# Kernel tuning notes

Measured on AMD Instinct MI355X. Metric: run time of the kernel, lower is better.

## Reference

```python
import jax, jax.numpy as jnp
import numpy as np

D_MODEL = 1024
NUM_HEADS = 16
D_K = D_MODEL // NUM_HEADS


def setup_inputs() -> dict:
    key = jax.random.key(0)
    ks = jax.random.split(key, 7)
    B, S = 4, 2048
    lim = float(np.sqrt(6.0 / (D_MODEL + D_MODEL)))  # xavier uniform
    x = jax.random.normal(ks[0], (B, S, D_MODEL), dtype=jnp.float32)
    w_q = jax.random.uniform(ks[1], (D_MODEL, D_MODEL), jnp.float32, -lim, lim)
    w_k = jax.random.uniform(ks[2], (D_MODEL, D_MODEL), jnp.float32, -lim, lim)
    w_v = jax.random.uniform(ks[3], (D_MODEL, D_MODEL), jnp.float32, -lim, lim)
    w_o = jax.random.uniform(ks[4], (D_MODEL, D_MODEL), jnp.float32, -lim, lim)
    b_o = jnp.zeros((D_MODEL,), jnp.float32)
    ln_g = jnp.ones((D_MODEL,), jnp.float32)
    ln_b = jnp.zeros((D_MODEL,), jnp.float32)
    return {"x": x, "w_q": w_q, "w_k": w_k, "w_v": w_v, "w_o": w_o,
            "b_o": b_o, "ln_g": ln_g, "ln_b": ln_b}


def _layer_norm(y, g, b, eps=1e-5):
    mu = jnp.mean(y, axis=-1, keepdims=True)
    var = jnp.var(y, axis=-1, keepdims=True)
    return (y - mu) * jax.lax.rsqrt(var + eps) * g + b


def reference(x, w_q, w_k, w_v, w_o, b_o, ln_g, ln_b):
    B, S, D = x.shape
    # Linear weights stored torch-style [out, in]: y = x @ W^T
    def proj(w):
        return jnp.einsum('bsd,ed->bse', x, w).reshape(B, S, NUM_HEADS, D_K).transpose(0, 2, 1, 3)
    Q, K, V = proj(w_q), proj(w_k), proj(w_v)  # [B, H, S, d_k]
    scores = jnp.einsum('bhqd,bhkd->bhqk', Q, K) / jnp.sqrt(jnp.float32(D_K))
    attn = jax.nn.softmax(scores, axis=-1)  # dropout identity at eval
    out = jnp.einsum('bhqk,bhkd->bhqd', attn, V)  # [B, H, S, d_k]
    out = out.transpose(0, 2, 1, 3).reshape(B, S, D)
    out = jnp.einsum('bsd,ed->bse', out, w_o) + b_o
    return _layer_norm(x + out, ln_g, ln_b)
```

## Files before the change

### kernel.cpp

```cpp
#include <hip/hip_runtime.h>

typedef __bf16 bf16;
typedef bf16 v8bf __attribute__((ext_vector_type(8)));
typedef bf16 v4bf __attribute__((ext_vector_type(4)));
typedef float v4f __attribute__((ext_vector_type(4)));
typedef float v16f __attribute__((ext_vector_type(16)));
typedef unsigned int u32;
typedef u32 v4u __attribute__((ext_vector_type(4)));

#define GAS __attribute__((address_space(1)))
#define LAS __attribute__((address_space(3)))

constexpr int D    = 1024;
constexpr int ROWS = 8192;
constexpr int TILE = 128;

__global__ __launch_bounds__(256) void cast_all(
    const float* __restrict__ x,
    const float* __restrict__ wq, const float* __restrict__ wk,
    const float* __restrict__ wv, const float* __restrict__ wo,
    bf16* __restrict__ xb, bf16* __restrict__ wqb, bf16* __restrict__ wkb,
    bf16* __restrict__ wvb, bf16* __restrict__ wob)
{
    int i = blockIdx.x * 256 + threadIdx.x;
    const float* src; bf16* dst; int off;
    if (i < 2 * 1024 * 1024) { src = x; dst = xb; off = i; }
    else {
        int j = i - 2 * 1024 * 1024;
        int w = j >> 18;
        off = j & ((1 << 18) - 1);
        src = (w == 0) ? wq : (w == 1) ? wk : (w == 2) ? wv : wo;
        dst = (w == 0) ? wqb : (w == 1) ? wkb : (w == 2) ? wvb : wob;
    }
    float4 v = ((const float4*)src)[off];
    v4bf o;
    o[0] = (bf16)v.x; o[1] = (bf16)v.y; o[2] = (bf16)v.z; o[3] = (bf16)v.w;
    ((v4bf*)dst)[off] = o;
}

template<int MODE>
__global__ __launch_bounds__(256) void gemm_bt(
    const bf16* __restrict__ A,
    const bf16* __restrict__ W0, const bf16* __restrict__ W1, const bf16* __restrict__ W2,
    bf16* __restrict__ O0, bf16* __restrict__ O1, bf16* __restrict__ O2,
    float* __restrict__ Of, const float* __restrict__ bias,
    const float* __restrict__ X)
{
    __shared__ bf16 As[2][TILE * 32];
    __shared__ bf16 Bs[2][TILE * 32];

    const int tid  = threadIdx.x;
    const int lane = tid & 63;
    const int wave = tid >> 6;
    const int quad = lane >> 4;
    const int l16  = lane & 15;
    const int wm   = (wave >> 1) * 64;
    const int wn   = (wave & 1) * 64;

    const int z = blockIdx.z;
    const bf16* Bw = (MODE == 0) ? ((z == 0) ? W0 : ((z == 1) ? W1 : W2)) : W0;
    bf16*       Ob = (MODE == 0) ? ((z == 0) ? O0 : ((z == 1) ? O1 : O2)) : O0;

    const long rowA0 = (long)blockIdx.y * TILE;
    const long rowB0 = (long)blockIdx.x * TILE;

    const int stRow = wave * 16 + (lane >> 2);
    const int stCol = (lane & 3) * 8;
    const bf16* gA = A  + (rowA0 + stRow) * D + stCol;
    const bf16* gB = Bw + (rowB0 + stRow) * D + stCol;
    const int ldsOff = wave * 16 * 32;

    const v4f vzero = {0.f, 0.f, 0.f, 0.f};
    v4f acc[4][4];
    #pragma unroll
    for (int i = 0; i < 4; i++)
        #pragma unroll
        for (int j = 0; j < 4; j++) acc[i][j] = vzero;

    for (int k0 = 0; k0 < D; k0 += 64) {
        __syncthreads();
        #pragma unroll
        for (int p = 0; p < 2; ++p)
            #pragma unroll
            for (int i = 0; i < 2; ++i) {
                __builtin_amdgcn_global_load_lds(
                    (const GAS void*)(gA + (long)i * 64 * D + p * 32),
                    (LAS void*)(&As[p][ldsOff + i * 64 * 32]), 16, 0, 0);
                __builtin_amdgcn_global_load_lds(
                    (const GAS void*)(gB + (long)i * 64 * D + p * 32),
                    (LAS void*)(&Bs[p][ldsOff + i * 64 * 32]), 16, 0, 0);
            }
        gA += 64; gB += 64;
        __syncthreads();

        #pragma unroll
        for (int p = 0; p < 2; ++p) {
            v8bf a[4], b[4];
            #pragma unroll
            for (int mi = 0; mi < 4; mi++)
                a[mi] = *(const v8bf*)(&As[p][(wm + mi * 16 + l16) * 32 + quad * 8]);
            #pragma unroll
            for (int ni = 0; ni < 4; ni++)
                b[ni] = *(const v8bf*)(&Bs[p][(wn + ni * 16 + l16) * 32 + quad * 8]);
            #pragma unroll
            for (int mi = 0; mi < 4; mi++)
                #pragma unroll
                for (int ni = 0; ni < 4; ni++)
                    acc[mi][ni] = __builtin_amdgcn_mfma_f32_16x16x32_bf16(a[mi], b[ni], acc[mi][ni], 0, 0, 0);
        }
    }

    const float qscale = 0.125f * 1.44269504f;

    if (MODE == 0 && z == 2) {
        #pragma unroll
        for (int mi = 0; mi < 4; mi++) {
            #pragma unroll
            for (int ni = 0; ni < 4; ni++) {
                const long col = rowB0 + wn + ni * 16 + l16;
                const long h_ = col >> 6, dd = col & 63;
                const long row0 = rowA0 + wm + mi * 16 + quad * 4;
                const long b_ = row0 >> 11, s0 = row0 & 2047;
                v4bf pk;
                #pragma unroll
                for (int r = 0; r < 4; r++) pk[r] = (bf16)acc[mi][ni][r];
                *(v4bf*)(Ob + ((b_ * 16 + h_) * 64 + dd) * 2048 + s0) = pk;
            }
        }
    } else {
        #pragma unroll
        for (int mi = 0; mi < 4; mi++) {
            #pragma unroll
            for (int ni = 0; ni < 4; ni++) {
                const long col = rowB0 + wn + ni * 16 + l16;
                float bv = (MODE == 1) ? bias[col] : 0.f;
                #pragma unroll
                for (int r = 0; r < 4; r++) {
                    const long row = rowA0 + wm + mi * 16 + quad * 4 + r;
                    float v = acc[mi][ni][r];
                    if (MODE == 1) Of[row * D + col] = v + bv + X[row * D + col];
                    else {
                        if (z == 0) v *= qscale;
                        Ob[row * D + col] = (bf16)v;
                    }
                }
            }
        }
    }
}

__global__ __launch_bounds__(256) void attn_kernel(
    const bf16* __restrict__ Q, const bf16* __restrict__ Kg,
    const bf16* __restrict__ VtG, bf16* __restrict__ O)
{
    const int qt = blockIdx.x, h = blockIdx.y, b = blockIdx.z;
    const int tid  = threadIdx.x;
    const int lane = tid & 63;
    const int wave = tid >> 6;
    const int l31  = lane & 31;
    const int hi   = lane >> 5;

    __shared__ bf16 Kt[64 * 64];
    __shared__ bf16 Vt[64 * 64];

    const long qrow = (long)(b * 2048 + qt * 128 + wave * 32 + l31);
    v8bf qB[4];
    #pragma unroll
    for (int f = 0; f < 4; f++)
        qB[f] = *(const v8bf*)(Q + qrow * D + h * 64 + f * 16 + hi * 8);

    v16f o_acc[2];
    #pragma unroll
    for (int d2 = 0; d2 < 2; d2++)
        #pragma unroll
        for (int i = 0; i < 16; i++) o_acc[d2][i] = 0.f;
    float l_acc = 0.f;

    const int iR = tid >> 3;
    const int c8 = tid & 7;
    const int sC = c8 * 8;
    const bf16* kLane = Kg  + (long)b * 2048 * D + h * 64 + sC + (long)iR * D;
    const bf16* vLane = VtG + (long)(b * 16 + h) * 64 * 2048 + sC + (long)iR * 2048;
    const int wOff = iR * 64 + ((c8 ^ (iR & 7)) * 8);
    bf16* ktW = Kt + wOff;
    bf16* vtW = Vt + wOff;

    v8bf kpre[2], vpre[2];
    kpre[0] = *(const v8bf*)(kLane);
    kpre[1] = *(const v8bf*)(kLane + 32 * D);
    vpre[0] = *(const v8bf*)(vLane);
    vpre[1] = *(const v8bf*)(vLane + 32 * 2048);
    kLane += 64 * D;
    vLane += 64;

    for (int kt = 0; kt < 32; ++kt) {
        __syncthreads();
        *(v8bf*)(ktW)            = kpre[0];
        *(v8bf*)(ktW + 32 * 64)  = kpre[1];
        *(v8bf*)(vtW)            = vpre[0];
        *(v8bf*)(vtW + 32 * 64)  = vpre[1];
        __syncthreads();

        if (kt + 1 < 32) {
            kpre[0] = *(const v8bf*)(kLane);
            kpre[1] = *(const v8bf*)(kLane + 32 * D);
            vpre[0] = *(const v8bf*)(vLane);
            vpre[1] = *(const v8bf*)(vLane + 32 * 2048);
            kLane += 64 * D;
            vLane += 64;
        }

        #pragma unroll
        for (int ko = 0; ko < 2; ko++) {
            v16f st;
            #pragma unroll
            for (int i = 0; i < 16; i++) st[i] = 0.f;
            const int krow = ko * 32 + l31;
            const int ksw  = krow & 7;
            #pragma unroll
            for (int f = 0; f < 4; f++) {
                v8bf kA = *(const v8bf*)(Kt + krow * 64 + (((2 * f + hi) ^ ksw) * 8));
                st = __builtin_amdgcn_mfma_f32_32x32x16_bf16(kA, qB[f], st, 0, 0, 0);
            }

            float p[16];
            #pragma unroll
            for (int r = 0; r < 16; r++) {
                p[r] = __builtin_amdgcn_exp2f(st[r]);
                l_acc += p[r];
            }

            #pragma unroll
            for (int u = 0; u < 2; u++) {
                const int s = ko * 2 + u;
                u32 a0, a1, b0, b1;
                asm("v_cvt_pk_bf16_f32 %0, %1, %2" : "=v"(a0) : "v"(p[u*8+0]), "v"(p[u*8+1]));
                asm("v_cvt_pk_bf16_f32 %0, %1, %2" : "=v"(a1) : "v"(p[u*8+2]), "v"(p[u*8+3]));
                asm("v_cvt_pk_bf16_f32 %0, %1, %2" : "=v"(b0) : "v"(p[u*8+4]), "v"(p[u*8+5]));
                asm("v_cvt_pk_bf16_f32 %0, %1, %2" : "=v"(b1) : "v"(p[u*8+6]), "v"(p[u*8+7]));
                asm("v_permlane32_swap_b32 %0, %1" : "+v"(a0), "+v"(b0));
                asm("v_permlane32_swap_b32 %0, %1" : "+v"(a1), "+v"(b1));
                v4u w; w[0] = a0; w[1] = a1; w[2] = b0; w[3] = b1;
                const v8bf pa = __builtin_bit_cast(v8bf, w);
                #pragma unroll
                for (int d2 = 0; d2 < 2; d2++) {
                    const int vrow = d2 * 32 + l31;
                    v8bf vb = *(const v8bf*)(Vt + vrow * 64 + (((2 * s + hi) ^ (vrow & 7)) * 8));
                    o_acc[d2] = __builtin_amdgcn_mfma_f32_32x32x16_bf16(pa, vb, o_acc[d2], 0, 0, 0);
                }
            }
        }
    }

    l_acc += __shfl_xor(l_acc, 32);

    const long obase = (long)(b * 2048 + qt * 128 + wave * 32);
    #pragma unroll
    for (int r = 0; r < 16; r++) {
        const int qp = (r & 3) + 8 * (r >> 2) + 4 * hi;
        const float inv = 1.f / __shfl(l_acc, qp);
        O[(obase + qp) * D + h * 64 + l31]      = (bf16)(o_acc[0][r] * inv);
        O[(obase + qp) * D + h * 64 + 32 + l31] = (bf16)(o_acc[1][r] * inv);
    }
}

__global__ __launch_bounds__(256) void ln_kernel(
    const float* __restrict__ g, const float* __restrict__ beta,
    float* __restrict__ out)
{
    const int row = blockIdx.x;
    const int t = threadIdx.x;
    const int lane = t & 63, wave = t >> 6;
    const long base = (long)row * D + t * 4;

    float4 yv = *(const float4*)(out + base);
    float y0 = yv.x, y1 = yv.y, y2 = yv.z, y3 = yv.w;
    float s1 = y0 + y1 + y2 + y3;
    float s2 = y0*y0 + y1*y1 + y2*y2 + y3*y3;
    #pragma unroll
    for (int off = 1; off < 64; off <<= 1) {
        s1 += __shfl_xor(s1, off);
        s2 += __shfl_xor(s2, off);
    }
    __shared__ float r1[4], r2[4];
    if (lane == 0) { r1[wave] = s1; r2[wave] = s2; }
    __syncthreads();
    float S1 = r1[0] + r1[1] + r1[2] + r1[3];
    float S2 = r2[0] + r2[1] + r2[2] + r2[3];
    float mu  = S1 * (1.f / 1024.f);
    float var = S2 * (1.f / 1024.f) - mu * mu;
    float rsd = rsqrtf(var + 1e-5f);

    float4 gv = *(const float4*)(g + t * 4);
    float4 bv = *(const float4*)(beta + t * 4);
    float4 o;
    o.x = (y0 - mu) * rsd * gv.x + bv.x;
    o.y = (y1 - mu) * rsd * gv.y + bv.y;
    o.z = (y2 - mu) * rsd * gv.z + bv.z;
    o.w = (y3 - mu) * rsd * gv.w + bv.w;
    *(float4*)(out + base) = o;
}

extern "C" void kernel_launch(void* const* d_in, const int* in_sizes, int n_in,
                              void* d_out, int out_size, void* d_ws, size_t ws_size,
                              hipStream_t stream)
{
    const float* x   = (const float*)d_in[0];
    const float* wq  = (const float*)d_in[1];
    const float* wk  = (const float*)d_in[2];
    const float* wv  = (const float*)d_in[3];
    const float* wo  = (const float*)d_in[4];
    const float* bo  = (const float*)d_in[5];
    const float* lng = (const float*)d_in[6];
    const float* lnb = (const float*)d_in[7];
    float* out = (float*)d_out;

    char* ws = (char*)d_ws;
    bf16* xb  = (bf16*)(ws);
    bf16* wqb = (bf16*)(ws + (size_t)16 * 1024 * 1024);
    bf16* wkb = wqb + 1024 * 1024;
    bf16* wvb = wkb + 1024 * 1024;
    bf16* wob = wvb + 1024 * 1024;
    bf16* Qb  = (bf16*)(ws + (size_t)24 * 1024 * 1024);
    bf16* Kb  = Qb + (size_t)ROWS * D;
    bf16* VtG = Kb + (size_t)ROWS * D;
    bf16* Ab  = VtG + (size_t)ROWS * D;

    cast_all<<<12288, 256, 0, stream>>>(x, wq, wk, wv, wo,
                                        xb, wqb, wkb, wvb, wob);

    dim3 gqkv(D / TILE, ROWS / TILE, 3);
    gemm_bt<0><<<gqkv, 256, 0, stream>>>(xb, wqb, wkb, wvb, Qb, Kb, VtG,
                                         nullptr, nullptr, nullptr);

    attn_kernel<<<dim3(16, 16, 4), 256, 0, stream>>>(Qb, Kb, VtG, Ab);

    dim3 gout(D / TILE, ROWS / TILE, 1);
    gemm_bt<1><<<gout, 256, 0, stream>>>(Ab, wob, nullptr, nullptr,
                                         nullptr, nullptr, nullptr, out, bo, x);

    ln_kernel<<<8192, 256, 0, stream>>>(lng, lnb, out);
}
```

Before: 310.9 us.

## Double-buffer attention K/V LDS tiles and remap blocks for XCD locality

The attention kernel now keeps two LDS buffers for the K and V tiles, so each iteration writes the next tile into the idle buffer while computing on the current one. This removes one of the two block barriers per iteration. The grid is flattened to 1D and remapped so that all 16 query tiles of a given (batch, head) land on the same XCD, which should improve L2 reuse of K/V. It also seeds the first MFMA with a zero accumulator and splits the row-sum into two partial sums to shorten dependency chains, at the cost of doubling LDS per block.

```diff
diff --git a/kernel.cpp b/kernel.cpp
--- a/kernel.cpp
+++ b/kernel.cpp
@@ -153,15 +153,20 @@
     const bf16* __restrict__ Q, const bf16* __restrict__ Kg,
     const bf16* __restrict__ VtG, bf16* __restrict__ O)
 {
-    const int qt = blockIdx.x, h = blockIdx.y, b = blockIdx.z;
+    const int id  = blockIdx.x;
+    const int xcd = id & 7, j = id >> 3;
+    const int qt  = j & 15;
+    const int g   = xcd + 8 * (j >> 4);
+    const int h   = g & 15, b = g >> 4;
+
     const int tid  = threadIdx.x;
     const int lane = tid & 63;
     const int wave = tid >> 6;
     const int l31  = lane & 31;
     const int hi   = lane >> 5;
 
-    __shared__ bf16 Kt[64 * 64];
-    __shared__ bf16 Vt[64 * 64];
+    __shared__ bf16 Kt[2][64 * 64];
+    __shared__ bf16 Vt[2][64 * 64];
 
     const long qrow = (long)(b * 2048 + qt * 128 + wave * 32 + l31);
     v8bf qB[4];
@@ -169,12 +174,11 @@
     for (int f = 0; f < 4; f++)
         qB[f] = *(const v8bf*)(Q + qrow * D + h * 64 + f * 16 + hi * 8);
 
+    const v16f z16 = {0.f,0.f,0.f,0.f,0.f,0.f,0.f,0.f,
+                      0.f,0.f,0.f,0.f,0.f,0.f,0.f,0.f};
     v16f o_acc[2];
-    #pragma unroll
-    for (int d2 = 0; d2 < 2; d2++)
-        #pragma unroll
-        for (int i = 0; i < 16; i++) o_acc[d2][i] = 0.f;
-    float l_acc = 0.f;
+    o_acc[0] = z16; o_acc[1] = z16;
+    float l0 = 0.f, l1 = 0.f;
 
     const int iR = tid >> 3;
     const int c8 = tid & 7;
@@ -182,44 +186,50 @@
     const bf16* kLane = Kg  + (long)b * 2048 * D + h * 64 + sC + (long)iR * D;
     const bf16* vLane = VtG + (long)(b * 16 + h) * 64 * 2048 + sC + (long)iR * 2048;
     const int wOff = iR * 64 + ((c8 ^ (iR & 7)) * 8);
-    bf16* ktW = Kt + wOff;
-    bf16* vtW = Vt + wOff;
 
     v8bf kpre[2], vpre[2];
     kpre[0] = *(const v8bf*)(kLane);
     kpre[1] = *(const v8bf*)(kLane + 32 * D);
     vpre[0] = *(const v8bf*)(vLane);
     vpre[1] = *(const v8bf*)(vLane + 32 * 2048);
-    kLane += 64 * D;
-    vLane += 64;
+    kLane += 64 * D; vLane += 64;
+    *(v8bf*)(&Kt[0][wOff])           = kpre[0];
+    *(v8bf*)(&Kt[0][wOff + 32 * 64]) = kpre[1];
+    *(v8bf*)(&Vt[0][wOff])           = vpre[0];
+    *(v8bf*)(&Vt[0][wOff + 32 * 64]) = vpre[1];
+    kpre[0] = *(const v8bf*)(kLane);
+    kpre[1] = *(const v8bf*)(kLane + 32 * D);
+    vpre[0] = *(const v8bf*)(vLane);
+    vpre[1] = *(const v8bf*)(vLane + 32 * 2048);
+    kLane += 64 * D; vLane += 64;
 
     for (int kt = 0; kt < 32; ++kt) {
+        const int cur = kt & 1;
         __syncthreads();
-        *(v8bf*)(ktW)            = kpre[0];
-        *(v8bf*)(ktW + 32 * 64)  = kpre[1];
-        *(v8bf*)(vtW)            = vpre[0];
-        *(v8bf*)(vtW + 32 * 64)  = vpre[1];
-        __syncthreads();
 
         if (kt + 1 < 32) {
+            *(v8bf*)(&Kt[cur ^ 1][wOff])           = kpre[0];
+            *(v8bf*)(&Kt[cur ^ 1][wOff + 32 * 64]) = kpre[1];
+            *(v8bf*)(&Vt[cur ^ 1][wOff])           = vpre[0];
+            *(v8bf*)(&Vt[cur ^ 1][wOff + 32 * 64]) = vpre[1];
+        }
+        if (kt + 2 < 32) {
             kpre[0] = *(const v8bf*)(kLane);
             kpre[1] = *(const v8bf*)(kLane + 32 * D);
             vpre[0] = *(const v8bf*)(vLane);
             vpre[1] = *(const v8bf*)(vLane + 32 * 2048);
-            kLane += 64 * D;
-            vLane += 64;
+            kLane += 64 * D; vLane += 64;
         }
 
         #pragma unroll
         for (int ko = 0; ko < 2; ko++) {
-            v16f st;
-            #pragma unroll
-            for (int i = 0; i < 16; i++) st[i] = 0.f;
             const int krow = ko * 32 + l31;
             const int ksw  = krow & 7;
-            #pragma unroll
-            for (int f = 0; f < 4; f++) {
-                v8bf kA = *(const v8bf*)(Kt + krow * 64 + (((2 * f + hi) ^ ksw) * 8));
+            v8bf kA0 = *(const v8bf*)(&Kt[cur][krow * 64 + (((0 + hi) ^ ksw) * 8)]);
+            v16f st  = __builtin_amdgcn_mfma_f32_32x32x16_bf16(kA0, qB[0], z16, 0, 0, 0);
+            #pragma unroll
+            for (int f = 1; f < 4; f++) {
+                v8bf kA = *(const v8bf*)(&Kt[cur][krow * 64 + (((2 * f + hi) ^ ksw) * 8)]);
                 st = __builtin_amdgcn_mfma_f32_32x32x16_bf16(kA, qB[f], st, 0, 0, 0);
             }
 
@@ -227,7 +237,7 @@
             #pragma unroll
             for (int r = 0; r < 16; r++) {
                 p[r] = __builtin_amdgcn_exp2f(st[r]);
-                l_acc += p[r];
+                if (r & 1) l1 += p[r]; else l0 += p[r];
             }
 
             #pragma unroll
@@ -245,13 +255,14 @@
                 #pragma unroll
                 for (int d2 = 0; d2 < 2; d2++) {
                     const int vrow = d2 * 32 + l31;
-                    v8bf vb = *(const v8bf*)(Vt + vrow * 64 + (((2 * s + hi) ^ (vrow & 7)) * 8));
+                    v8bf vb = *(const v8bf*)(&Vt[cur][vrow * 64 + (((2 * s + hi) ^ (vrow & 7)) * 8)]);
                     o_acc[d2] = __builtin_amdgcn_mfma_f32_32x32x16_bf16(pa, vb, o_acc[d2], 0, 0, 0);
                 }
             }
         }
     }
 
+    float l_acc = l0 + l1;
     l_acc += __shfl_xor(l_acc, 32);
 
     const long obase = (long)(b * 2048 + qt * 128 + wave * 32);
@@ -333,7 +344,7 @@
     gemm_bt<0><<<gqkv, 256, 0, stream>>>(xb, wqb, wkb, wvb, Qb, Kb, VtG,
                                          nullptr, nullptr, nullptr);
 
-    attn_kernel<<<dim3(16, 16, 4), 256, 0, stream>>>(Qb, Kb, VtG, Ab);
+    attn_kernel<<<dim3(1024, 1, 1), 256, 0, stream>>>(Qb, Kb, VtG, Ab);
 
     dim3 gout(D / TILE, ROWS / TILE, 1);
     gemm_bt<1><<<gout, 256, 0, stream>>>(Ab, wob, nullptr, nullptr,
```

Measured after the change: 299.9 us. 1.04x faster.
